# Optimization experiments

Measured on AMD Instinct MI355X. Metric: run time of the kernel, lower is better.

The kernel has to match this reference:

```python
import jax, jax.numpy as jnp
import numpy as np

NITERS = 5  # mean-field iterations (niters in __init__)


def setup_inputs() -> dict:
    key = jax.random.key(0)
    k1, k2 = jax.random.split(key)
    B, L, C, H, W = 2, 21, 3, 96, 96
    E0 = jax.random.normal(k1, (B, L, H, W), dtype=jnp.float32)
    Refs = jax.random.normal(k2, (B, C, H, W), dtype=jnp.float32)
    # potts_init: weight = ones(L,L) - eye(L)
    Mu_W = jnp.ones((L, L), dtype=jnp.float32) - jnp.eye(L, dtype=jnp.float32)
    return {"E0": E0, "Refs": Refs, "Mu_W": Mu_W}


def _affinity(Refs):
    # Reference-guided dense adjacency (BatchedAdjacency): row-normalized
    # Gaussian affinity on guide features, one N x N matrix per batch element.
    B, C, H, W = Refs.shape
    N = H * W
    f = Refs.reshape(B, C, N).transpose(0, 2, 1)  # [B, N, C]
    sq = jnp.sum(f * f, axis=-1)  # [B, N]
    D = sq[:, :, None] + sq[:, None, :] - 2.0 * jnp.einsum('bnc,bmc->bnm', f, f)
    A = jnp.exp(-0.5 * D)  # [B, N, N]
    return A / jnp.sum(A, axis=-1, keepdims=True)


def reference(E0, Refs, Mu_W):
    B, L, H, W = E0.shape
    N = H * W
    A = _affinity(Refs)  # computed once, reused every iteration
    E0f = E0.reshape(B, L, N)
    Qf = jax.nn.softmax(-E0f, axis=1)  # Q = softmax(-E0, dim=1)
    for _ in range(NITERS):
        # Potts compatibility transform (channel mixing): Mu(Q)
        M = jnp.einsum('kl,bln->bkn', Mu_W, Qf)
        # adjacency message passing: W(Mu(Q), Refs)
        msg = jnp.einsum('bnm,blm->bln', A, M)
        Qf = jax.nn.softmax(-(E0f + msg), axis=1)
    return Qf.reshape(B, L, H, W)
```

## Files before the change

kernel.cpp:

```cpp
#include <hip/hip_runtime.h>
#include <hip/hip_bf16.h>


#define BB 2
#define LL 21
#define LP (LL + 1)
#define NNPX 9216
#define NITERS 5
#define MSPLIT 8
#define LOG2E 1.4426950408889634f

#define BARRIER() asm volatile("s_waitcnt lgkmcnt(0)\n\ts_barrier" ::: "memory")

typedef __attribute__((ext_vector_type(8))) short short8;
typedef __attribute__((ext_vector_type(4))) float f32x4;

static __device__ inline unsigned int pk_bf16(float a, float b) {
    __hip_bfloat162 h = __float22bfloat162_rn(make_float2(a, b));
    unsigned int u;
    __builtin_memcpy(&u, &h, 4);
    return u;
}

__global__ __launch_bounds__(256) void k_prep(
        const float* __restrict__ E0, const float* __restrict__ Refs,
        const float* __restrict__ Mu,
        float4* __restrict__ FN, float4* __restrict__ FS,
        __hip_bfloat16* __restrict__ MQ) {
    __shared__ float muS[LL * LL];
    for (int i = threadIdx.x; i < LL * LL; i += 256) muS[i] = Mu[i];
    __syncthreads();

    int idx = blockIdx.x * 256 + threadIdx.x;
    int b = idx / NNPX, n = idx % NNPX;

    const float* rb = Refs + (size_t)b * 3 * NNPX + n;
    float r0 = rb[0], r1 = rb[NNPX], r2 = rb[2 * NNPX];
    FN[idx] = make_float4(r0, r1, r2, 0.f);
    float g = -0.5f * (r0 * r0 + r1 * r1 + r2 * r2);
    FS[idx] = make_float4(g * LOG2E, r0 * LOG2E, r1 * LOG2E, r2 * LOG2E);

    const float* eb = E0 + (size_t)b * LL * NNPX + n;
    float x[LL];
    float mx = -1e30f;
    for (int l = 0; l < LL; ++l) { x[l] = -eb[(size_t)l * NNPX]; mx = fmaxf(mx, x[l]); }
    float s = 0.f;
    for (int l = 0; l < LL; ++l) { x[l] = __builtin_amdgcn_exp2f((x[l] - mx) * LOG2E); s += x[l]; }
    float rs = __builtin_amdgcn_rcpf(s);
    for (int l = 0; l < LL; ++l) x[l] *= rs;

    __hip_bfloat16* mq = MQ + (size_t)b * LL * NNPX + n;
    for (int k = 0; k < LL; ++k) {
        float a = 0.f;
        for (int l = 0; l < LL; ++l) a += muS[k * LL + l] * x[l];
        mq[(size_t)k * NNPX] = __float2bfloat16(a);
    }
}

__global__ __launch_bounds__(256, 4) void k_accum(
        const float4* __restrict__ FS, const float4* __restrict__ FN,
        const unsigned int* __restrict__ MQbf, float* __restrict__ Ppart) {
    __shared__ __align__(16) unsigned short Wlds[64 * 64];
    __shared__ __align__(16) unsigned short Mlds[32 * 72];

    int t = threadIdx.x;
    int rb = blockIdx.x;
    int s  = blockIdx.y;
    int b  = rb / 144;
    int n0 = (rb % 144) * 64;
    int wv = t >> 6, lane = t & 63;
    int lr = lane & 15, g = lane >> 4;

    for (int i = t; i < 11 * 32; i += 256) {
        int r = 21 + (i >> 5), d = i & 31;
        ((unsigned int*)&Mlds[r * 72])[d] = (r == 21) ? 0x3F803F80u : 0u;
    }

    int mq = t & 15;
    int ng = t >> 4;
    float fnx[4], fny[4], fnz[4];
    #pragma unroll
    for (int i = 0; i < 4; ++i) {
        float4 v = FN[b * NNPX + n0 + ng + 16 * i];
        fnx[i] = v.x; fny[i] = v.y; fnz[i] = v.z;
    }

    const int T  = 144 / MSPLIT;
    const int t0 = s * T;
    const float4* fsb = FS + (size_t)b * NNPX;
    const unsigned int* mqb = MQbf + (size_t)b * LL * (NNPX / 2);

    int sl0 = t >> 5, sm0 = t & 31;
    int sl1 = (t + 256) >> 5, sm1 = (t + 256) & 31;
    int sl2 = (t + 512) >> 5, sm2 = (t + 512) & 31;

    f32x4 acc0 = {0.f, 0.f, 0.f, 0.f};
    f32x4 acc1 = {0.f, 0.f, 0.f, 0.f};

    int wcol = (((mq >> 1) ^ (ng & 7)) << 3) + ((mq & 1) << 2);

    int row = wv * 16 + lr;
    int ia0 = row * 64 + ((g ^ (lr & 7)) << 3);
    int ia1 = row * 64 + (((g + 4) ^ (lr & 7)) << 3);

    float4 fsA0, fsA1, fsA2, fsA3;
    unsigned int mrA0, mrA1, mrA2;

    auto LOAD = [&](int tile) {
        int m0 = (t0 + tile) * 64;
        fsA0 = fsb[m0 + 4 * mq + 0]; fsA1 = fsb[m0 + 4 * mq + 1];
        fsA2 = fsb[m0 + 4 * mq + 2]; fsA3 = fsb[m0 + 4 * mq + 3];
        int mo0 = (t0 + tile) * 32;
        mrA0 = mqb[(size_t)sl0 * (NNPX / 2) + mo0 + sm0];
        mrA1 = mqb[(size_t)sl1 * (NNPX / 2) + mo0 + sm1];
        if (t < 160) mrA2 = mqb[(size_t)sl2 * (NNPX / 2) + mo0 + sm2];
    };
    auto STORE = [&]() {
        ((unsigned int*)&Mlds[sl0 * 72])[sm0] = mrA0;
        ((unsigned int*)&Mlds[sl1 * 72])[sm1] = mrA1;
        if (t < 160) ((unsigned int*)&Mlds[sl2 * 72])[sm2] = mrA2;
        #pragma unroll
        for (int i = 0; i < 4; ++i) {
            float w0 = __builtin_amdgcn_exp2f(fsA0.x + fnx[i] * fsA0.y + fny[i] * fsA0.z + fnz[i] * fsA0.w);
            float w1 = __builtin_amdgcn_exp2f(fsA1.x + fnx[i] * fsA1.y + fny[i] * fsA1.z + fnz[i] * fsA1.w);
            float w2 = __builtin_amdgcn_exp2f(fsA2.x + fnx[i] * fsA2.y + fny[i] * fsA2.z + fnz[i] * fsA2.w);
            float w3 = __builtin_amdgcn_exp2f(fsA3.x + fnx[i] * fsA3.y + fny[i] * fsA3.z + fnz[i] * fsA3.w);
            uint2 pk;
            pk.x = pk_bf16(w0, w1);
            pk.y = pk_bf16(w2, w3);
            *(uint2*)&Wlds[(ng + 16 * i) * 64 + wcol] = pk;
        }
    };
    auto MFMA = [&]() {
        short8 a0  = *(const short8*)&Wlds[ia0];
        short8 a1  = *(const short8*)&Wlds[ia1];
        short8 b00 = *(const short8*)&Mlds[lr * 72 + g * 8];
        short8 b01 = *(const short8*)&Mlds[lr * 72 + g * 8 + 32];
        short8 b10 = *(const short8*)&Mlds[(16 + lr) * 72 + g * 8];
        short8 b11 = *(const short8*)&Mlds[(16 + lr) * 72 + g * 8 + 32];
        acc0 = __builtin_amdgcn_mfma_f32_16x16x32_bf16(a0, b00, acc0, 0, 0, 0);
        acc0 = __builtin_amdgcn_mfma_f32_16x16x32_bf16(a1, b01, acc0, 0, 0, 0);
        acc1 = __builtin_amdgcn_mfma_f32_16x16x32_bf16(a0, b10, acc1, 0, 0, 0);
        acc1 = __builtin_amdgcn_mfma_f32_16x16x32_bf16(a1, b11, acc1, 0, 0, 0);
    };

    LOAD(0);

    for (int tt = 0; tt < T; ++tt) {
        BARRIER();
        STORE();
        if (tt + 1 < T) LOAD(tt + 1);
        BARRIER();
        MFMA();
    }

    int col = lane & 15, qr = lane >> 4;
    float* pp = Ppart + (size_t)b * LP * NNPX;
    for (int r = 0; r < 4; ++r) {
        int n = n0 + wv * 16 + qr * 4 + r;
        atomicAdd(&pp[(size_t)col * NNPX + n], acc0[r]);
        if (col < LP - 16) atomicAdd(&pp[(size_t)(16 + col) * NNPX + n], acc1[r]);
    }
}

template <bool LAST>
__global__ __launch_bounds__(256) void k_softmax(
        const float* __restrict__ E0, const float* __restrict__ Ppart,
        const float* __restrict__ Mu,
        __hip_bfloat16* __restrict__ MQ, float* __restrict__ Out) {
    __shared__ float muS[LL * LL];
    for (int i = threadIdx.x; i < LL * LL; i += 256) muS[i] = Mu[i];
    __syncthreads();

    int idx = blockIdx.x * 256 + threadIdx.x;
    int b = idx / NNPX, n = idx % NNPX;

    const float* pp = Ppart + (size_t)b * LP * NNPX + n;
    float rinv = __builtin_amdgcn_rcpf(pp[(size_t)LL * NNPX]);

    const float* eb = E0 + (size_t)b * LL * NNPX + n;
    float P[LL];
    float mx = -1e30f;
    for (int l = 0; l < LL; ++l) {
        P[l] = -(eb[(size_t)l * NNPX] + pp[(size_t)l * NNPX] * rinv);
        mx = fmaxf(mx, P[l]);
    }
    float ssum = 0.f;
    for (int l = 0; l < LL; ++l) { P[l] = __builtin_amdgcn_exp2f((P[l] - mx) * LOG2E); ssum += P[l]; }
    float rs = __builtin_amdgcn_rcpf(ssum);
    for (int l = 0; l < LL; ++l) P[l] *= rs;

    if (LAST) {
        float* ob = Out + (size_t)b * LL * NNPX + n;
        for (int l = 0; l < LL; ++l) ob[(size_t)l * NNPX] = P[l];
    } else {
        __hip_bfloat16* mq = MQ + (size_t)b * LL * NNPX + n;
        for (int k = 0; k < LL; ++k) {
            float a = 0.f;
            for (int l = 0; l < LL; ++l) a += muS[k * LL + l] * P[l];
            mq[(size_t)k * NNPX] = __float2bfloat16(a);
        }
    }
}

extern "C" void kernel_launch(void* const* d_in, const int* in_sizes, int n_in,
                              void* d_out, int out_size, void* d_ws, size_t ws_size,
                              hipStream_t stream) {
    const float* E0   = (const float*)d_in[0];
    const float* Refs = (const float*)d_in[1];
    const float* Mu   = (const float*)d_in[2];
    float* out = (float*)d_out;

    char* w = (char*)d_ws;
    size_t off = 0;
    auto alloc = [&](size_t bytes) {
        void* p = w + off;
        off += (bytes + 255) & ~(size_t)255;
        return p;
    };
    float4* FN     = (float4*)alloc((size_t)BB * NNPX * sizeof(float4));
    float4* FS     = (float4*)alloc((size_t)BB * NNPX * sizeof(float4));
    __hip_bfloat16* MQbf = (__hip_bfloat16*)alloc((size_t)BB * LL * NNPX * sizeof(__hip_bfloat16));
    size_t psz = (size_t)BB * LP * NNPX * sizeof(float);
    float* Ppart = (float*)alloc(psz);

    k_prep<<<BB * NNPX / 256, 256, 0, stream>>>(E0, Refs, Mu, FN, FS, MQbf);
    for (int it = 0; it < NITERS; ++it) {
        hipMemsetAsync(Ppart, 0, psz, stream);
        k_accum<<<dim3(288, MSPLIT), 256, 0, stream>>>(FS, FN, (const unsigned int*)MQbf, Ppart);
        if (it == NITERS - 1)
            k_softmax<true><<<BB * NNPX / 256, 256, 0, stream>>>(E0, Ppart, Mu, MQbf, out);
        else
            k_softmax<false><<<BB * NNPX / 256, 256, 0, stream>>>(E0, Ppart, Mu, MQbf, out);
    }
}
```

Measured before the change: 423.8 us.

## Replace atomic split-K accumulation with per-split partial buffers and parallelize softmax kernels

Result: faster. 387.3 us (-8.6%).

```diff
diff --git a/kernel.cpp b/kernel.cpp
--- a/kernel.cpp
+++ b/kernel.cpp
@@ -7,7 +7,6 @@
 #define LP (LL + 1)
 #define NNPX 9216
 #define NITERS 5
-#define MSPLIT 8
 #define LOG2E 1.4426950408889634f
 
 #define BARRIER() asm volatile("s_waitcnt lgkmcnt(0)\n\ts_barrier" ::: "memory")
@@ -28,40 +27,64 @@
         float4* __restrict__ FN, float4* __restrict__ FS,
         __hip_bfloat16* __restrict__ MQ) {
     __shared__ float muS[LL * LL];
-    for (int i = threadIdx.x; i < LL * LL; i += 256) muS[i] = Mu[i];
-    __syncthreads();
-
-    int idx = blockIdx.x * 256 + threadIdx.x;
-    int b = idx / NNPX, n = idx % NNPX;
-
-    const float* rb = Refs + (size_t)b * 3 * NNPX + n;
-    float r0 = rb[0], r1 = rb[NNPX], r2 = rb[2 * NNPX];
-    FN[idx] = make_float4(r0, r1, r2, 0.f);
-    float g = -0.5f * (r0 * r0 + r1 * r1 + r2 * r2);
-    FS[idx] = make_float4(g * LOG2E, r0 * LOG2E, r1 * LOG2E, r2 * LOG2E);
-
+    __shared__ float red1[4][64], red2[4][64];
+    __shared__ float Qs[LL][64];
+
+    int t = threadIdx.x;
+    for (int i = t; i < LL * LL; i += 256) muS[i] = Mu[i];
+
+    int q = t >> 6, px = t & 63;
+    int pid = blockIdx.x * 64 + px;
+    int b = pid / NNPX, n = pid % NNPX;
+
+    if (q == 0) {
+        const float* rb = Refs + (size_t)b * 3 * NNPX + n;
+        float r0 = rb[0], r1 = rb[NNPX], r2 = rb[2 * NNPX];
+        FN[pid] = make_float4(r0, r1, r2, 0.f);
+        float g = -0.5f * (r0 * r0 + r1 * r1 + r2 * r2);
+        FS[pid] = make_float4(g * LOG2E, r0 * LOG2E, r1 * LOG2E, r2 * LOG2E);
+    }
+
+    int l0 = q * 6;
     const float* eb = E0 + (size_t)b * LL * NNPX + n;
-    float x[LL];
+    float x[6];
     float mx = -1e30f;
-    for (int l = 0; l < LL; ++l) { x[l] = -eb[(size_t)l * NNPX]; mx = fmaxf(mx, x[l]); }
+    #pragma unroll
+    for (int i = 0; i < 6; ++i) {
+        int l = l0 + i;
+        x[i] = (l < LL) ? -eb[(size_t)l * NNPX] : -1e30f;
+        mx = fmaxf(mx, x[i]);
+    }
+    red1[q][px] = mx;
+    __syncthreads();
+    mx = fmaxf(fmaxf(red1[0][px], red1[1][px]), fmaxf(red1[2][px], red1[3][px]));
     float s = 0.f;
-    for (int l = 0; l < LL; ++l) { x[l] = __builtin_amdgcn_exp2f((x[l] - mx) * LOG2E); s += x[l]; }
-    float rs = __builtin_amdgcn_rcpf(s);
-    for (int l = 0; l < LL; ++l) x[l] *= rs;
+    #pragma unroll
+    for (int i = 0; i < 6; ++i) { x[i] = __builtin_amdgcn_exp2f((x[i] - mx) * LOG2E); s += x[i]; }
+    red2[q][px] = s;
+    __syncthreads();
+    float rs = __builtin_amdgcn_rcpf(red2[0][px] + red2[1][px] + red2[2][px] + red2[3][px]);
+    #pragma unroll
+    for (int i = 0; i < 6; ++i) if (l0 + i < LL) Qs[l0 + i][px] = x[i] * rs;
+    __syncthreads();
 
     __hip_bfloat16* mq = MQ + (size_t)b * LL * NNPX + n;
-    for (int k = 0; k < LL; ++k) {
-        float a = 0.f;
-        for (int l = 0; l < LL; ++l) a += muS[k * LL + l] * x[l];
-        mq[(size_t)k * NNPX] = __float2bfloat16(a);
+    #pragma unroll
+    for (int j = 0; j < 6; ++j) {
+        int k = l0 + j;
+        if (k < LL) {
+            float a = 0.f;
+            for (int l = 0; l < LL; ++l) a += muS[k * LL + l] * Qs[l][px];
+            mq[(size_t)k * NNPX] = __float2bfloat16(a);
+        }
     }
 }
 
 __global__ __launch_bounds__(256, 4) void k_accum(
         const float4* __restrict__ FS, const float4* __restrict__ FN,
-        const unsigned int* __restrict__ MQbf, float* __restrict__ Ppart) {
+        const unsigned int* __restrict__ MQbf, float* __restrict__ Ppart, int S) {
     __shared__ __align__(16) unsigned short Wlds[64 * 64];
-    __shared__ __align__(16) unsigned short Mlds[32 * 72];
+    __shared__ __align__(16) unsigned short Mlds[32 * 64];
 
     int t = threadIdx.x;
     int rb = blockIdx.x;
@@ -73,7 +96,7 @@
 
     for (int i = t; i < 11 * 32; i += 256) {
         int r = 21 + (i >> 5), d = i & 31;
-        ((unsigned int*)&Mlds[r * 72])[d] = (r == 21) ? 0x3F803F80u : 0u;
+        ((unsigned int*)&Mlds[r * 64])[d] = (r == 21) ? 0x3F803F80u : 0u;
     }
 
     int mq = t & 15;
@@ -85,7 +108,7 @@
         fnx[i] = v.x; fny[i] = v.y; fnz[i] = v.z;
     }
 
-    const int T  = 144 / MSPLIT;
+    const int T  = 144 / S;
     const int t0 = s * T;
     const float4* fsb = FS + (size_t)b * NNPX;
     const unsigned int* mqb = MQbf + (size_t)b * LL * (NNPX / 2);
@@ -93,6 +116,9 @@
     int sl0 = t >> 5, sm0 = t & 31;
     int sl1 = (t + 256) >> 5, sm1 = (t + 256) & 31;
     int sl2 = (t + 512) >> 5, sm2 = (t + 512) & 31;
+    int mw0 = sl0 * 32 + (((sm0 >> 2) ^ (sl0 & 7)) << 2) + (sm0 & 3);
+    int mw1 = sl1 * 32 + (((sm1 >> 2) ^ (sl1 & 7)) << 2) + (sm1 & 3);
+    int mw2 = sl2 * 32 + (((sm2 >> 2) ^ (sl2 & 7)) << 2) + (sm2 & 3);
 
     f32x4 acc0 = {0.f, 0.f, 0.f, 0.f};
     f32x4 acc1 = {0.f, 0.f, 0.f, 0.f};
@@ -102,6 +128,10 @@
     int row = wv * 16 + lr;
     int ia0 = row * 64 + ((g ^ (lr & 7)) << 3);
     int ia1 = row * 64 + (((g + 4) ^ (lr & 7)) << 3);
+    int ib0 = lr * 64 + ((g ^ (lr & 7)) << 3);
+    int ib1 = lr * 64 + (((g + 4) ^ (lr & 7)) << 3);
+    int ib2 = (16 + lr) * 64 + ((g ^ (lr & 7)) << 3);
+    int ib3 = (16 + lr) * 64 + (((g + 4) ^ (lr & 7)) << 3);
 
     float4 fsA0, fsA1, fsA2, fsA3;
     unsigned int mrA0, mrA1, mrA2;
@@ -116,9 +146,9 @@
         if (t < 160) mrA2 = mqb[(size_t)sl2 * (NNPX / 2) + mo0 + sm2];
     };
     auto STORE = [&]() {
-        ((unsigned int*)&Mlds[sl0 * 72])[sm0] = mrA0;
-        ((unsigned int*)&Mlds[sl1 * 72])[sm1] = mrA1;
-        if (t < 160) ((unsigned int*)&Mlds[sl2 * 72])[sm2] = mrA2;
+        ((unsigned int*)Mlds)[mw0] = mrA0;
+        ((unsigned int*)Mlds)[mw1] = mrA1;
+        if (t < 160) ((unsigned int*)Mlds)[mw2] = mrA2;
         #pragma unroll
         for (int i = 0; i < 4; ++i) {
             float w0 = __builtin_amdgcn_exp2f(fsA0.x + fnx[i] * fsA0.y + fny[i] * fsA0.z + fnz[i] * fsA0.w);
@@ -134,10 +164,10 @@
     auto MFMA = [&]() {
         short8 a0  = *(const short8*)&Wlds[ia0];
         short8 a1  = *(const short8*)&Wlds[ia1];
-        short8 b00 = *(const short8*)&Mlds[lr * 72 + g * 8];
-        short8 b01 = *(const short8*)&Mlds[lr * 72 + g * 8 + 32];
-        short8 b10 = *(const short8*)&Mlds[(16 + lr) * 72 + g * 8];
-        short8 b11 = *(const short8*)&Mlds[(16 + lr) * 72 + g * 8 + 32];
+        short8 b00 = *(const short8*)&Mlds[ib0];
+        short8 b01 = *(const short8*)&Mlds[ib1];
+        short8 b10 = *(const short8*)&Mlds[ib2];
+        short8 b11 = *(const short8*)&Mlds[ib3];
         acc0 = __builtin_amdgcn_mfma_f32_16x16x32_bf16(a0, b00, acc0, 0, 0, 0);
         acc0 = __builtin_amdgcn_mfma_f32_16x16x32_bf16(a1, b01, acc0, 0, 0, 0);
         acc1 = __builtin_amdgcn_mfma_f32_16x16x32_bf16(a0, b10, acc1, 0, 0, 0);
@@ -155,11 +185,11 @@
     }
 
     int col = lane & 15, qr = lane >> 4;
-    float* pp = Ppart + (size_t)b * LP * NNPX;
+    float* pp = Ppart + ((size_t)(s * BB + b) * LP) * NNPX;
     for (int r = 0; r < 4; ++r) {
         int n = n0 + wv * 16 + qr * 4 + r;
-        atomicAdd(&pp[(size_t)col * NNPX + n], acc0[r]);
-        if (col < LP - 16) atomicAdd(&pp[(size_t)(16 + col) * NNPX + n], acc1[r]);
+        pp[(size_t)col * NNPX + n] = acc0[r];
+        if (col < LP - 16) pp[(size_t)(16 + col) * NNPX + n] = acc1[r];
     }
 }
 
@@ -167,38 +197,77 @@
 __global__ __launch_bounds__(256) void k_softmax(
         const float* __restrict__ E0, const float* __restrict__ Ppart,
         const float* __restrict__ Mu,
-        __hip_bfloat16* __restrict__ MQ, float* __restrict__ Out) {
+        __hip_bfloat16* __restrict__ MQ, float* __restrict__ Out, int S) {
     __shared__ float muS[LL * LL];
-    for (int i = threadIdx.x; i < LL * LL; i += 256) muS[i] = Mu[i];
-    __syncthreads();
-
-    int idx = blockIdx.x * 256 + threadIdx.x;
-    int b = idx / NNPX, n = idx % NNPX;
-
-    const float* pp = Ppart + (size_t)b * LP * NNPX + n;
-    float rinv = __builtin_amdgcn_rcpf(pp[(size_t)LL * NNPX]);
-
+    __shared__ float rsumS[64];
+    __shared__ float red1[4][64], red2[4][64];
+    __shared__ float Qs[LL][64];
+
+    int t = threadIdx.x;
+    if (!LAST) for (int i = t; i < LL * LL; i += 256) muS[i] = Mu[i];
+
+    int q = t >> 6, px = t & 63;
+    int pid = blockIdx.x * 64 + px;
+    int b = pid / NNPX, n = pid % NNPX;
+
+    int l0 = q * 6;
+    const float* ppb = Ppart + n;
     const float* eb = E0 + (size_t)b * LL * NNPX + n;
-    float P[LL];
+
+    float Pa[6], e0v[6];
+    #pragma unroll
+    for (int i = 0; i < 6; ++i) {
+        int l = l0 + i;
+        Pa[i] = 0.f; e0v[i] = 0.f;
+        if (l < LL) {
+            for (int s = 0; s < S; ++s)
+                Pa[i] += ppb[((size_t)(s * BB + b) * LP + l) * NNPX];
+            e0v[i] = eb[(size_t)l * NNPX];
+        }
+    }
+    if (q == 3) {
+        float racc = 0.f;
+        for (int s = 0; s < S; ++s)
+            racc += ppb[((size_t)(s * BB + b) * LP + LL) * NNPX];
+        rsumS[px] = racc;
+    }
+    __syncthreads();
+    float rinv = __builtin_amdgcn_rcpf(rsumS[px]);
+
+    float x[6];
     float mx = -1e30f;
-    for (int l = 0; l < LL; ++l) {
-        P[l] = -(eb[(size_t)l * NNPX] + pp[(size_t)l * NNPX] * rinv);
-        mx = fmaxf(mx, P[l]);
-    }
+    #pragma unroll
+    for (int i = 0; i < 6; ++i) {
+        x[i] = (l0 + i < LL) ? -(e0v[i] + Pa[i] * rinv) : -1e30f;
+        mx = fmaxf(mx, x[i]);
+    }
+    red1[q][px] = mx;
+    __syncthreads();
+    mx = fmaxf(fmaxf(red1[0][px], red1[1][px]), fmaxf(red1[2][px], red1[3][px]));
     float ssum = 0.f;
-    for (int l = 0; l < LL; ++l) { P[l] = __builtin_amdgcn_exp2f((P[l] - mx) * LOG2E); ssum += P[l]; }
-    float rs = __builtin_amdgcn_rcpf(ssum);
-    for (int l = 0; l < LL; ++l) P[l] *= rs;
+    #pragma unroll
+    for (int i = 0; i < 6; ++i) { x[i] = __builtin_amdgcn_exp2f((x[i] - mx) * LOG2E); ssum += x[i]; }
+    red2[q][px] = ssum;
+    __syncthreads();
+    float rs = __builtin_amdgcn_rcpf(red2[0][px] + red2[1][px] + red2[2][px] + red2[3][px]);
 
     if (LAST) {
         float* ob = Out + (size_t)b * LL * NNPX + n;
-        for (int l = 0; l < LL; ++l) ob[(size_t)l * NNPX] = P[l];
+        #pragma unroll
+        for (int i = 0; i < 6; ++i) if (l0 + i < LL) ob[(size_t)(l0 + i) * NNPX] = x[i] * rs;
     } else {
+        #pragma unroll
+        for (int i = 0; i < 6; ++i) if (l0 + i < LL) Qs[l0 + i][px] = x[i] * rs;
+        __syncthreads();
         __hip_bfloat16* mq = MQ + (size_t)b * LL * NNPX + n;
-        for (int k = 0; k < LL; ++k) {
-            float a = 0.f;
-            for (int l = 0; l < LL; ++l) a += muS[k * LL + l] * P[l];
-            mq[(size_t)k * NNPX] = __float2bfloat16(a);
+        #pragma unroll
+        for (int j = 0; j < 6; ++j) {
+            int k = l0 + j;
+            if (k < LL) {
+                float a = 0.f;
+                for (int l = 0; l < LL; ++l) a += muS[k * LL + l] * Qs[l][px];
+                mq[(size_t)k * NNPX] = __float2bfloat16(a);
+            }
         }
     }
 }
@@ -221,16 +290,21 @@
     float4* FN     = (float4*)alloc((size_t)BB * NNPX * sizeof(float4));
     float4* FS     = (float4*)alloc((size_t)BB * NNPX * sizeof(float4));
     __hip_bfloat16* MQbf = (__hip_bfloat16*)alloc((size_t)BB * LL * NNPX * sizeof(__hip_bfloat16));
-    size_t psz = (size_t)BB * LP * NNPX * sizeof(float);
-    float* Ppart = (float*)alloc(psz);
-
-    k_prep<<<BB * NNPX / 256, 256, 0, stream>>>(E0, Refs, Mu, FN, FS, MQbf);
+
+    size_t per = (size_t)BB * LP * NNPX * sizeof(float);
+    size_t avail = ws_size > off ? ws_size - off : 0;
+    int Smax = (int)(avail / (per + 256));
+    static const int divs[] = {8, 6, 4, 3, 2, 1};
+    int S = 1;
+    for (int i = 0; i < 6; ++i) if (divs[i] <= Smax) { S = divs[i]; break; }
+    float* Ppart = (float*)alloc((size_t)S * per);
+
+    k_prep<<<BB * NNPX / 64, 256, 0, stream>>>(E0, Refs, Mu, FN, FS, MQbf);
     for (int it = 0; it < NITERS; ++it) {
-        hipMemsetAsync(Ppart, 0, psz, stream);
-        k_accum<<<dim3(288, MSPLIT), 256, 0, stream>>>(FS, FN, (const unsigned int*)MQbf, Ppart);
+        k_accum<<<dim3(288, S), 256, 0, stream>>>(FS, FN, (const unsigned int*)MQbf, Ppart, S);
         if (it == NITERS - 1)
-            k_softmax<true><<<BB * NNPX / 256, 256, 0, stream>>>(E0, Ppart, Mu, MQbf, out);
+            k_softmax<true><<<BB * NNPX / 64, 256, 0, stream>>>(E0, Ppart, Mu, MQbf, out, S);
         else
-            k_softmax<false><<<BB * NNPX / 256, 256, 0, stream>>>(E0, Ppart, Mu, MQbf, out);
-    }
-}
+            k_softmax<false><<<BB * NNPX / 64, 256, 0, stream>>>(E0, Ppart, Mu, MQbf, out, S);
+    }
+}
```
